# Optimization experiments

Measured on AMD Instinct MI355X. Metric: run time of the kernel, lower is better.

## Reference

```python
import jax, jax.numpy as jnp
import numpy as np


def _dwconv(x, w, b):
    # depthwise conv, NCHW, kernel [C,1,k,k], SAME padding k//2
    k = w.shape[-1]
    p = k // 2
    out = jax.lax.conv_general_dilated(x, w, (1, 1), [(p, p), (p, p)],
                                       feature_group_count=x.shape[1])
    return out + b[None, :, None, None]


def _conv1x1(x, W, b):
    return jnp.einsum('oc,bchw->bohw', W, x) + b[None, :, None, None]


def _ca_weight(q, k):
    # q,k: [b,c,h,w] -> energy [b,h,w,h+w]
    eH = jnp.einsum('bchw,bcgw->bhwg', q, k)  # attend along H (column)
    eW = jnp.einsum('bchw,bchv->bhwv', q, k)  # attend along W (row)
    return jnp.concatenate([eH, eW], axis=3)


def _ca_map(att, v):
    # att: [b,h,w,h+w], v: [b,c,h,w]
    h = v.shape[2]
    outH = jnp.einsum('bcgw,bhwg->bchw', v, att[..., :h])
    outW = jnp.einsum('bchv,bhwv->bchw', v, att[..., h:])
    return outH + outW


def _cc_block(cnn, Wq, bq, Wk, bk, Wv, bv, gamma):
    q = _conv1x1(cnn, Wq, bq)
    k = _conv1x1(cnn, Wk, bk)
    v = _conv1x1(cnn, Wv, bv)
    att = jax.nn.softmax(_ca_weight(q, k), axis=1)  # softmax over H axis, as in torch F.softmax(energy, 1)
    return gamma * _ca_map(att, v) + cnn


def _ppeg(x, w7, b7, w5, b5, w3, b3, H, W):
    C = x.shape[1]
    cnn = x.T.reshape(1, C, H, W)
    out = _dwconv(cnn, w7, b7) + cnn + _dwconv(cnn, w5, b5) + _dwconv(cnn, w3, b3)
    return out.reshape(C, H * W).T  # [N, C]


def setup_inputs() -> dict:
    key = jax.random.key(0)
    N, DIM, HID, QK = 65536, 1024, 512, 64  # N = 256^2
    ks = jax.random.split(key, 26)
    s = 0.02
    inp = {
        'h0': jax.random.normal(ks[0], (N, DIM), jnp.float32),
        'w7': jax.random.normal(ks[1], (DIM, 1, 7, 7)) * s,
        'b7': jax.random.normal(ks[2], (DIM,)) * s,
        'w5': jax.random.normal(ks[3], (DIM, 1, 5, 5)) * s,
        'b5': jax.random.normal(ks[4], (DIM,)) * s,
        'w3': jax.random.normal(ks[5], (DIM, 1, 3, 3)) * s,
        'b3': jax.random.normal(ks[6], (DIM,)) * s,
        'W1': jax.random.normal(ks[7], (HID, DIM)) * s,
        'b1': jax.random.normal(ks[8], (HID,)) * s,
        'Wq': jax.random.normal(ks[9], (QK, HID)) * s,
        'bq': jax.random.normal(ks[10], (QK,)) * s,
        'Wk': jax.random.normal(ks[11], (QK, HID)) * s,
        'bk': jax.random.normal(ks[12], (QK,)) * s,
        'Wv': jax.random.normal(ks[13], (HID, HID)) * s,
        'bv': jax.random.normal(ks[14], (HID,)) * s,
        'gamma': jax.random.normal(ks[15], ()) * 0.5,
        'Wq1': jax.random.normal(ks[16], (QK, HID)) * s,
        'bq1': jax.random.normal(ks[17], (QK,)) * s,
        'Wk1': jax.random.normal(ks[18], (QK, HID)) * s,
        'bk1': jax.random.normal(ks[19], (QK,)) * s,
        'Wv1': jax.random.normal(ks[20], (HID, HID)) * s,
        'bv1': jax.random.normal(ks[21], (HID,)) * s,
        'gamma1': jax.random.normal(ks[22], ()) * 0.5,
        'Wfc': jax.random.normal(ks[23], (1, HID)) * s,
        'bfc': jax.random.normal(ks[24], (1,)) * s,
    }
    return inp


def reference(h0, w7, b7, w5, b5, w3, b3, W1, b1,
              Wq, bq, Wk, bk, Wv, bv, gamma,
              Wq1, bq1, Wk1, bk1, Wv1, bv1, gamma1, Wfc, bfc):
    N = h0.shape[0]
    side = int(np.ceil(np.sqrt(N)))
    pad = side * side - N
    h1 = jnp.concatenate([h0, h0[:pad]], axis=0) if pad > 0 else h0
    # PPEG positional encoding (multi-kernel depthwise conv)
    h1 = _ppeg(h1, w7, b7, w5, b5, w3, b3, side, side)
    # fc1: Linear(1024->512) + ReLU  (h1 already square -> second pad is no-op)
    h2 = jax.nn.relu(h1 @ W1.T + b1)  # [N, 512]
    # CCAttention (two criss-cross blocks + fc to 1 logit)
    cnn = h2.T.reshape(1, h2.shape[1], side, side)
    out = _cc_block(cnn, Wq, bq, Wk, bk, Wv, bv, gamma)
    out1 = _cc_block(out, Wq1, bq1, Wk1, bk1, Wv1, bv1, gamma1)
    out1 = out1.reshape(out1.shape[1], side * side).T  # [N, 512]
    logits = out1 @ Wfc.T + bfc  # [N, 1]
    A = jax.nn.softmax(logits.T, axis=1)  # [1, N] attention over instances
    return A
```

## Files before the change

### kernel.cpp

```cpp
#include <hip/hip_runtime.h>

#define HW 65536
#define SIDE 256

typedef __attribute__((ext_vector_type(8))) short short8v;
typedef __attribute__((ext_vector_type(4))) float f32x4;
typedef __attribute__((ext_vector_type(8))) ushort ushort8v;

__device__ __forceinline__ ushort f2bf(float f) {
  unsigned int u = __builtin_bit_cast(unsigned int, f);
  u = (u + 0x7fff + ((u >> 16) & 1)) >> 16;
  return (ushort)u;
}
__device__ __forceinline__ float bf2f(unsigned int u) {
  return __builtin_bit_cast(float, (u & 0xffffu) << 16);
}
__device__ __forceinline__ float bflo(unsigned int d) {
  return __builtin_bit_cast(float, d << 16);
}
__device__ __forceinline__ float bfhi(unsigned int d) {
  return __builtin_bit_cast(float, d & 0xffff0000u);
}
__device__ __forceinline__ void gld16(const void* g, void* l) {
  __builtin_amdgcn_global_load_lds(
      (const __attribute__((address_space(1))) void*)g,
      (__attribute__((address_space(3))) void*)l, 16, 0, 0);
}

__global__ __launch_bounds__(256) void k_prep(
    const float* __restrict__ W1, const float* __restrict__ Wv,
    const float* __restrict__ Wv1, const float* __restrict__ Wq,
    const float* __restrict__ Wk, const float* __restrict__ Wq1,
    const float* __restrict__ Wk1, const float* __restrict__ bq,
    const float* __restrict__ bk, const float* __restrict__ bq1,
    const float* __restrict__ bk1, const float* __restrict__ w7,
    const float* __restrict__ b7, const float* __restrict__ w5,
    const float* __restrict__ b5, const float* __restrict__ w3,
    const float* __restrict__ b3,
    ushort* __restrict__ W1b, ushort* __restrict__ Wvb,
    ushort* __restrict__ Wv1b, ushort* __restrict__ Wqkb,
    ushort* __restrict__ Wqk1b, float* __restrict__ bqk,
    float* __restrict__ bqk1, float* __restrict__ wc, float* __restrict__ bc) {
  const int i = blockIdx.x * 256 + threadIdx.x;
  if (i < 524288) { W1b[i] = f2bf(W1[i]); return; }
  if (i < 786432) { int j = i - 524288; Wvb[j] = f2bf(Wv[j]); return; }
  if (i < 1048576) { int j = i - 786432; Wv1b[j] = f2bf(Wv1[j]); return; }
  if (i < 1081344) { int j = i - 1048576; Wqkb[j] = f2bf(Wq[j]); return; }
  if (i < 1114112) { int j = i - 1081344; Wqkb[32768 + j] = f2bf(Wk[j]); return; }
  if (i < 1146880) { int j = i - 1114112; Wqk1b[j] = f2bf(Wq1[j]); return; }
  if (i < 1179648) { int j = i - 1146880; Wqk1b[32768 + j] = f2bf(Wk1[j]); return; }
  if (i < 1179904) {
    int j = i - 1179648;
    if (j < 64) bqk[j] = bq[j];
    else if (j < 128) bqk[j] = bk[j - 64];
    else if (j < 192) bqk1[j - 128] = bq1[j - 128];
    else bqk1[j - 128] = bk1[j - 192];
    return;
  }
  if (i < 1180928) {
    const int c = i - 1179904;
    float w[49];
#pragma unroll
    for (int t = 0; t < 49; t++) w[t] = w7[c * 49 + t];
    for (int dy = 0; dy < 5; dy++)
      for (int dx = 0; dx < 5; dx++)
        w[(dy + 1) * 7 + (dx + 1)] += w5[c * 25 + dy * 5 + dx];
    for (int dy = 0; dy < 3; dy++)
      for (int dx = 0; dx < 3; dx++)
        w[(dy + 2) * 7 + (dx + 2)] += w3[c * 9 + dy * 3 + dx];
    w[3 * 7 + 3] += 1.0f;
#pragma unroll
    for (int t = 0; t < 49; t++) wc[c * 49 + t] = w[t];
    bc[c] = b7[c] + b5[c] + b3[c];
  }
}

__global__ __launch_bounds__(256) void k_transpose_nc_v(
    const float* __restrict__ in, ushort* __restrict__ out) {
  __shared__ ushort t[64][64];
  const int c0 = blockIdx.x << 6, r0 = blockIdx.y << 6;
  const int tid = threadIdx.x;
#pragma unroll
  for (int p = 0; p < 2; p++) {
    const int r = (tid >> 3) + p * 32, c8 = tid & 7;
    const float4 f0 = *(const float4*)&in[(size_t)(r0 + r) * 1024 + c0 + c8 * 8];
    const float4 f1 = *(const float4*)&in[(size_t)(r0 + r) * 1024 + c0 + c8 * 8 + 4];
    ushort8v v;
    v[0] = f2bf(f0.x); v[1] = f2bf(f0.y); v[2] = f2bf(f0.z); v[3] = f2bf(f0.w);
    v[4] = f2bf(f1.x); v[5] = f2bf(f1.y); v[6] = f2bf(f1.z); v[7] = f2bf(f1.w);
    *(ushort8v*)&t[r][(c8 ^ ((r >> 3) & 7)) * 8] = v;
  }
  __syncthreads();
#pragma unroll
  for (int p = 0; p < 2; p++) {
    const int c = (tid >> 3) + p * 32, r8 = tid & 7;
    ushort8v v;
#pragma unroll
    for (int j = 0; j < 8; j++) {
      const int rr = r8 * 8 + j;
      v[j] = t[rr][(((c >> 3) ^ r8) << 3) + (c & 7)];
    }
    *(ushort8v*)&out[(size_t)(c0 + c) * HW + r0 + r8 * 8] = v;
  }
}

__global__ __launch_bounds__(256) void k_trv(const ushort* __restrict__ in,
    ushort* __restrict__ out, int R, int C, long long bs) {
  __shared__ ushort t[64][64];
  const size_t base = (size_t)blockIdx.z * bs;
  const int c0 = blockIdx.x << 6, r0 = blockIdx.y << 6;
  const int tid = threadIdx.x;
#pragma unroll
  for (int p = 0; p < 2; p++) {
    const int r = (tid >> 3) + p * 32, c8 = tid & 7;
    const ushort8v v = *(const ushort8v*)&in[base + (size_t)(r0 + r) * C + c0 + c8 * 8];
    *(ushort8v*)&t[r][(c8 ^ ((r >> 3) & 7)) * 8] = v;
  }
  __syncthreads();
#pragma unroll
  for (int p = 0; p < 2; p++) {
    const int c = (tid >> 3) + p * 32, r8 = tid & 7;
    ushort8v v;
#pragma unroll
    for (int j = 0; j < 8; j++) {
      const int rr = r8 * 8 + j;
      v[j] = t[rr][(((c >> 3) ^ r8) << 3) + (c & 7)];
    }
    *(ushort8v*)&out[base + (size_t)(c0 + c) * R + r0 + r8 * 8] = v;
  }
}

__global__ __launch_bounds__(256) void k_dwconv7(const ushort* __restrict__ X,
    const float* __restrict__ wc, const float* __restrict__ bc,
    ushort* __restrict__ out) {
  __shared__ ushort tile[38][272];
  const int c = blockIdx.y;
  const int y0 = blockIdx.x << 5;
  const int tid = threadIdx.x;
  const ushort* Xc = X + (size_t)c * HW;

  float w[49];
#pragma unroll
  for (int i = 0; i < 49; i++) w[i] = wc[c * 49 + i];
  const float bcv = bc[c];

  if (tid < 76) {
    const int r = tid >> 1;
    ushort8v z = {0, 0, 0, 0, 0, 0, 0, 0};
    *(ushort8v*)&tile[r][(tid & 1) ? 264 : 0] = z;
  }
  for (int i = tid; i < 38 * 32; i += 256) {
    const int r = i >> 5, j8 = i & 31;
    const int y = y0 - 3 + r;
    ushort8v v = {0, 0, 0, 0, 0, 0, 0, 0};
    if (y >= 0 && y < SIDE) v = *(const ushort8v*)&Xc[y * SIDE + j8 * 8];
    *(ushort8v*)&tile[r][8 + j8 * 8] = v;
  }
  __syncthreads();

  const int t0 = tid & 63;
  const int ry = (tid >> 6) << 3;
  float acc[8][4] = {};
#pragma unroll
  for (int r = 0; r < 14; r++) {
    const uint2 ua = *(const uint2*)&tile[ry + r][(t0 << 2) + 4];
    const uint2 ub = *(const uint2*)&tile[ry + r][(t0 << 2) + 8];
    const uint2 uc = *(const uint2*)&tile[ry + r][(t0 << 2) + 12];
    float rv[12];
    rv[0] = bflo(ua.x); rv[1] = bfhi(ua.x); rv[2] = bflo(ua.y); rv[3] = bfhi(ua.y);
    rv[4] = bflo(ub.x); rv[5] = bfhi(ub.x); rv[6] = bflo(ub.y); rv[7] = bfhi(ub.y);
    rv[8] = bflo(uc.x); rv[9] = bfhi(uc.x); rv[10] = bflo(uc.y); rv[11] = bfhi(uc.y);
#pragma unroll
    for (int m = 0; m < 8; m++) {
      const int dy = r - m;
      if (dy < 0 || dy > 6) continue;
#pragma unroll
      for (int dx = 0; dx < 7; dx++) {
        const float ww = w[dy * 7 + dx];
#pragma unroll
        for (int o = 0; o < 4; o++) acc[m][o] += ww * rv[o + 1 + dx];
      }
    }
  }
#pragma unroll
  for (int m = 0; m < 8; m++) {
    ushort4 o4 = {f2bf(acc[m][0] + bcv), f2bf(acc[m][1] + bcv),
                  f2bf(acc[m][2] + bcv), f2bf(acc[m][3] + bcv)};
    *(ushort4*)&out[(size_t)c * HW + (y0 + ry + m) * SIDE + (t0 << 2)] = o4;
  }
}

template <int BN, int BIAS, int RELU, int OUTF, int OUTB>
__global__ __launch_bounds__(256) void k_mm(
    const ushort* __restrict__ A, int lda, long long bsA,
    const ushort* __restrict__ B, int ldb, long long bsB,
    const float* __restrict__ bias,
    float* __restrict__ Cf, ushort* __restrict__ Cb, int ldc, long long bsC,
    int K) {
  static_assert(BN == 64 || BN == 128, "BN");
  constexpr int FN = BN / 32;
  __shared__ __align__(16) ushort As[128 * 32];
  __shared__ __align__(16) ushort Bs[BN * 32];
  const int tid = threadIdx.x;
  const int bm = blockIdx.x << 7, bn = blockIdx.y * BN;
  const long long zA = (long long)blockIdx.z * bsA;
  const long long zB = (long long)blockIdx.z * bsB;
  const long long zC = (long long)blockIdx.z * bsC;

  const int sr = tid >> 2, sq = tid & 3;
  const int sw0 = (sr >> 1) & 3;
  const int sw1 = ((sr + 64) >> 1) & 3;
  const ushort* Ap0 = A + zA + (size_t)(bm + sr) * lda + ((sq ^ sw0) << 3);
  const ushort* Ap1 = A + zA + (size_t)(bm + sr + 64) * lda + ((sq ^ sw1) << 3);
  const ushort* Bp0 = B + zB + (size_t)(bn + sr) * ldb + ((sq ^ sw0) << 3);
  const ushort* Bp1 = nullptr;
  if constexpr (BN == 128)
    Bp1 = B + zB + (size_t)(bn + sr + 64) * ldb + ((sq ^ sw1) << 3);
  ushort* wA0 = &As[sr * 32 + sq * 8];
  ushort* wA1 = &As[(sr + 64) * 32 + sq * 8];
  ushort* wB0 = &Bs[sr * 32 + sq * 8];
  ushort* wB1 = nullptr;
  if constexpr (BN == 128) wB1 = &Bs[(sr + 64) * 32 + sq * 8];

  const int lane = tid & 63, wv = tid >> 6;
  const int wm = wv & 1, wn = wv >> 1;
  const int fr = lane & 15, kq = lane >> 4;
  int offA[4], offB[FN];
#pragma unroll
  for (int mi = 0; mi < 4; mi++) {
    const int row = wm * 64 + mi * 16 + fr;
    offA[mi] = row * 32 + ((kq ^ ((row >> 1) & 3)) << 3);
  }
#pragma unroll
  for (int ni = 0; ni < FN; ni++) {
    const int row = wn * (BN / 2) + ni * 16 + fr;
    offB[ni] = row * 32 + ((kq ^ ((row >> 1) & 3)) << 3);
  }

  f32x4 acc[4][FN];
#pragma unroll
  for (int mi = 0; mi < 4; mi++)
#pragma unroll
    for (int ni = 0; ni < FN; ni++) acc[mi][ni] = (f32x4){0.f, 0.f, 0.f, 0.f};

  for (int k0 = 0; k0 < K; k0 += 32) {
    __syncthreads();
    gld16(Ap0 + k0, wA0);
    gld16(Ap1 + k0, wA1);
    gld16(Bp0 + k0, wB0);
    if constexpr (BN == 128) gld16(Bp1 + k0, wB1);
    __syncthreads();
    short8v a[4], b[FN];
#pragma unroll
    for (int mi = 0; mi < 4; mi++) a[mi] = *(const short8v*)&As[offA[mi]];
#pragma unroll
    for (int ni = 0; ni < FN; ni++) b[ni] = *(const short8v*)&Bs[offB[ni]];
#pragma unroll
    for (int mi = 0; mi < 4; mi++)
#pragma unroll
      for (int ni = 0; ni < FN; ni++)
        acc[mi][ni] = __builtin_amdgcn_mfma_f32_16x16x32_bf16(b[ni], a[mi], acc[mi][ni], 0, 0, 0);
  }

#pragma unroll
  for (int mi = 0; mi < 4; mi++) {
    const int row = bm + wm * 64 + mi * 16 + fr;
    const float bs1 = (BIAS == 1) ? bias[row] : 0.f;
#pragma unroll
    for (int ni = 0; ni < FN; ni++) {
      const int col = bn + wn * (BN / 2) + ni * 16 + (kq << 2);
      float4 v;
      v.x = acc[mi][ni][0]; v.y = acc[mi][ni][1];
      v.z = acc[mi][ni][2]; v.w = acc[mi][ni][3];
      if (BIAS == 1) { v.x += bs1; v.y += bs1; v.z += bs1; v.w += bs1; }
      if (BIAS == 2) {
        const float4 bc4 = *(const float4*)&bias[col];
        v.x += bc4.x; v.y += bc4.y; v.z += bc4.z; v.w += bc4.w;
      }
      if (RELU) {
        v.x = fmaxf(v.x, 0.f); v.y = fmaxf(v.y, 0.f);
        v.z = fmaxf(v.z, 0.f); v.w = fmaxf(v.w, 0.f);
      }
      const size_t idx = (size_t)(zC + (size_t)row * ldc + col);
      if (OUTF) *(float4*)&Cf[idx] = v;
      if (OUTB) {
        ushort4 u = {f2bf(v.x), f2bf(v.y), f2bf(v.z), f2bf(v.w)};
        *(ushort4*)&Cb[idx] = u;
      }
    }
  }
}

__global__ __launch_bounds__(256) void k_softmax_bf16(const ushort* __restrict__ E,
    ushort* __restrict__ Att, int outerStride, int hStride) {
  const size_t base = (size_t)blockIdx.x * outerStride + threadIdx.x;
  float m = -3.4e38f, s = 0.f;
  for (int h = 0; h < 256; h++) {
    const float x = bf2f(E[base + (size_t)h * hStride]);
    const float nm = fmaxf(m, x);
    s = s * __expf(m - nm) + __expf(x - nm);
    m = nm;
  }
  const float inv = 1.0f / s;
  for (int h = 0; h < 256; h++) {
    const size_t i = base + (size_t)h * hStride;
    Att[i] = f2bf(__expf(bf2f(E[i]) - m) * inv);
  }
}

__global__ __launch_bounds__(256) void k_merge3(const ushort* __restrict__ O,
    const ushort* __restrict__ TH, const ushort* __restrict__ CN,
    const float* __restrict__ gammap, ushort* __restrict__ outB) {
  __shared__ ushort t[64][64];
  const float g = *gammap;
  const size_t base = (size_t)blockIdx.z * HW;
  const int h0 = blockIdx.y << 6, w0 = blockIdx.x << 6;
  const int tid = threadIdx.x;
#pragma unroll
  for (int p = 0; p < 2; p++) {
    const int r = (tid >> 3) + p * 32, c8 = tid & 7;
    const ushort8v v = *(const ushort8v*)&TH[base + (w0 + r) * SIDE + h0 + c8 * 8];
    *(ushort8v*)&t[r][(c8 ^ ((r >> 3) & 7)) * 8] = v;
  }
  __syncthreads();
#pragma unroll
  for (int p = 0; p < 2; p++) {
    const int h = (tid >> 3) + p * 32, r8 = tid & 7;
    const size_t idx = base + (h0 + h) * SIDE + w0 + r8 * 8;
    const ushort8v o8 = *(const ushort8v*)&O[idx];
    const ushort8v c8v = *(const ushort8v*)&CN[idx];
    ushort8v res;
#pragma unroll
    for (int j = 0; j < 8; j++) {
      const int rr = r8 * 8 + j;
      const float th = bf2f(t[rr][(((h >> 3) ^ r8) << 3) + (h & 7)]);
      res[j] = f2bf(g * (bf2f(o8[j]) + th) + bf2f(c8v[j]));
    }
    *(ushort8v*)&outB[idx] = res;
  }
}

__global__ __launch_bounds__(256) void k_logits(const ushort* __restrict__ X,
    const float* __restrict__ Wfc, const float* __restrict__ bfc,
    float* __restrict__ L) {
  const int n = blockIdx.x * 256 + threadIdx.x;
  float s = 0.f;
  for (int j = 0; j < 512; j++) s += bf2f(X[(size_t)j * HW + n]) * Wfc[j];
  L[n] = s + bfc[0];
}

__global__ __launch_bounds__(256) void k_smax_reduce(const float* __restrict__ L,
                                                     float* __restrict__ red) {
  __shared__ float sm[256];
  const int tid = threadIdx.x;
  float m = -3.4e38f;
  for (int i = tid; i < HW; i += 256) m = fmaxf(m, L[i]);
  sm[tid] = m;
  __syncthreads();
  for (int s = 128; s > 0; s >>= 1) {
    if (tid < s) sm[tid] = fmaxf(sm[tid], sm[tid + s]);
    __syncthreads();
  }
  const float M = sm[0];
  __syncthreads();
  float sum = 0.f;
  for (int i = tid; i < HW; i += 256) sum += expf(L[i] - M);
  sm[tid] = sum;
  __syncthreads();
  for (int s = 128; s > 0; s >>= 1) {
    if (tid < s) sm[tid] += sm[tid + s];
    __syncthreads();
  }
  if (tid == 0) { red[0] = M; red[1] = sm[0]; }
}

__global__ __launch_bounds__(256) void k_smax_write(const float* __restrict__ L,
    const float* __restrict__ red, float* __restrict__ out) {
  const int n = blockIdx.x * 256 + threadIdx.x;
  out[n] = expf(L[n] - red[0]) * (1.0f / red[1]);
}

extern "C" void kernel_launch(void* const* d_in, const int* in_sizes, int n_in,
                              void* d_out, int out_size, void* d_ws, size_t ws_size,
                              hipStream_t stream) {
  const float* h0 = (const float*)d_in[0];
  const float* w7 = (const float*)d_in[1];
  const float* b7 = (const float*)d_in[2];
  const float* w5 = (const float*)d_in[3];
  const float* b5 = (const float*)d_in[4];
  const float* w3 = (const float*)d_in[5];
  const float* b3 = (const float*)d_in[6];
  const float* W1 = (const float*)d_in[7];
  const float* b1 = (const float*)d_in[8];
  const float* Wq = (const float*)d_in[9];
  const float* bq = (const float*)d_in[10];
  const float* Wk = (const float*)d_in[11];
  const float* bk = (const float*)d_in[12];
  const float* Wv = (const float*)d_in[13];
  const float* bv = (const float*)d_in[14];
  const float* gamma = (const float*)d_in[15];
  const float* Wq1 = (const float*)d_in[16];
  const float* bq1 = (const float*)d_in[17];
  const float* Wk1 = (const float*)d_in[18];
  const float* bk1 = (const float*)d_in[19];
  const float* Wv1 = (const float*)d_in[20];
  const float* bv1 = (const float*)d_in[21];
  const float* gamma1 = (const float*)d_in[22];
  const float* Wfc = (const float*)d_in[23];
  const float* bfc = (const float*)d_in[24];

  char* W = (char*)d_ws;
  const size_t MB = 1 << 20;
  ushort* Xb    = (ushort*)(W + 0);
  ushort* H2b   = (ushort*)(W + 0);
  ushort* H2t   = (ushort*)(W + 64 * MB);
  ushort* qkt   = (ushort*)(W + 128 * MB);
  ushort* AttW  = (ushort*)(W + 144 * MB);
  ushort* AttH  = (ushort*)(W + 176 * MB);
  ushort* H1b   = (ushort*)(W + 256 * MB);
  ushort* H1t   = (ushort*)(W + 384 * MB);
  ushort* Vb    = (ushort*)(W + 384 * MB);
  ushort* vTb   = (ushort*)(W + 448 * MB);
  ushort* Ob    = (ushort*)(W + 512 * MB);
  ushort* THbb  = (ushort*)(W + 576 * MB);
  ushort* Eb    = (ushort*)(W + 640 * MB);
  ushort* W1b   = (ushort*)(W + 704 * MB);
  ushort* Wvb   = (ushort*)(W + 705 * MB);
  ushort* Wv1b  = (ushort*)(W + 705 * MB + 512 * 1024);
  ushort* Wqkb  = (ushort*)(W + 706 * MB);
  ushort* Wqk1b = (ushort*)(W + 706 * MB + 128 * 1024);
  float*  wcomb = (float*)(W + 706 * MB + 256 * 1024);
  float*  bcomb = (float*)(W + 706 * MB + 464 * 1024);
  float*  bqk   = (float*)(W + 706 * MB + 472 * 1024);
  float*  bqk1  = (float*)(W + 706 * MB + 474 * 1024);
  float*  L     = (float*)(W + 707 * MB);
  float*  red   = (float*)(W + 707 * MB + 256 * 1024);

  k_prep<<<4613, 256, 0, stream>>>(W1, Wv, Wv1, Wq, Wk, Wq1, Wk1,
                                   bq, bk, bq1, bk1, w7, b7, w5, b5, w3, b3,
                                   W1b, Wvb, Wv1b, Wqkb, Wqk1b, bqk, bqk1,
                                   wcomb, bcomb);

  k_transpose_nc_v<<<dim3(16, 1024), 256, 0, stream>>>(h0, Xb);
  k_dwconv7<<<dim3(8, 1024), 256, 0, stream>>>(Xb, wcomb, bcomb, H1b);
  k_trv<<<dim3(1024, 16, 1), 256, 0, stream>>>(H1b, H1t, 1024, HW, 0);

  k_mm<128, 1, 1, 0, 1><<<dim3(4, 512, 1), 256, 0, stream>>>(
      W1b, 1024, 0, H1t, 1024, 0, b1, nullptr, H2b, HW, 0, 1024);
  k_trv<<<dim3(1024, 8, 1), 256, 0, stream>>>(H2b, H2t, 512, HW, 0);

  auto cc_block = [&](const ushort* act, ushort* cnn, const ushort* Wqk_,
                      const float* bqk_, const ushort* Wv_, const float* bv_,
                      const float* gam) {
    k_mm<128, 2, 0, 0, 1><<<dim3(512, 1, 1), 256, 0, stream>>>(
        act, 512, 0, Wqk_, 512, 0, bqk_, nullptr, qkt, 128, 0, 512);
    k_mm<128, 1, 0, 0, 1><<<dim3(4, 512, 1), 256, 0, stream>>>(
        Wv_, 512, 0, act, 512, 0, bv_, nullptr, Vb, HW, 0, 512);
    k_trv<<<dim3(4, 4, 512), 256, 0, stream>>>(Vb, vTb, 256, 256, 65536);
    k_mm<128, 0, 0, 0, 1><<<dim3(2, 2, 256), 256, 0, stream>>>(
        qkt, 128, 32768, qkt + 64, 128, 32768, nullptr, nullptr, Eb, 256, 65536, 64);
    k_softmax_bf16<<<256, 256, 0, stream>>>(Eb, AttW, 256, HW);
    k_mm<128, 0, 0, 0, 1><<<dim3(4, 2, 256), 256, 0, stream>>>(
        Vb, HW, 256, AttW, 256, 65536, nullptr, nullptr, Ob, HW, 256, 256);
    k_mm<128, 0, 0, 0, 1><<<dim3(2, 2, 256), 256, 0, stream>>>(
        qkt, 32768, 128, qkt + 64, 32768, 128, nullptr, nullptr, Eb, 256, 65536, 64);
    k_softmax_bf16<<<256, 256, 0, stream>>>(Eb, AttH, HW, 256);
    k_mm<128, 0, 0, 0, 1><<<dim3(4, 2, 256), 256, 0, stream>>>(
        vTb, HW, 256, AttH, 256, 65536, nullptr, nullptr, THbb, HW, 256, 256);
    k_merge3<<<dim3(4, 4, 512), 256, 0, stream>>>(Ob, THbb, cnn, gam, cnn);
  };

  cc_block(H2t, H2b, Wqkb, bqk, Wvb, bv, gamma);
  k_trv<<<dim3(1024, 8, 1), 256, 0, stream>>>(H2b, H2t, 512, HW, 0);
  cc_block(H2t, H2b, Wqk1b, bqk1, Wv1b, bv1, gamma1);

  k_logits<<<256, 256, 0, stream>>>(H2b, Wfc, bfc, L);
  k_smax_reduce<<<1, 256, 0, stream>>>(L, red);
  k_smax_write<<<256, 256, 0, stream>>>(L, red, (float*)d_out);
}
```

Baseline: 1.348 ms.

## Fuse transpose into fc1 GEMM, swizzle block order, merge both softmaxes

Adds a transposed-output epilogue to the GEMM: the tile is staged through shared memory so fc1 writes both H2b and H2t in one pass, which drops a separate transpose kernel. Adds XCD-aware block-index swizzles to several GEMM launches so that blocks sharing operands land on the same die's L2. The two softmax launches become one kernel over both energy buffers, which now get separate workspace areas so both energy GEMMs can run before it. The price is extra LDS traffic and syncs in the fc1 epilogue, plus a larger energy workspace.

```diff
diff --git a/kernel.cpp b/kernel.cpp
--- a/kernel.cpp
+++ b/kernel.cpp
@@ -190,22 +190,39 @@
   }
 }
 
-template <int BN, int BIAS, int RELU, int OUTF, int OUTB>
+template <int BN, int BIAS, int RELU, int OUTF, int OUTB, int SWZ, int TRN>
 __global__ __launch_bounds__(256) void k_mm(
     const ushort* __restrict__ A, int lda, long long bsA,
     const ushort* __restrict__ B, int ldb, long long bsB,
     const float* __restrict__ bias,
     float* __restrict__ Cf, ushort* __restrict__ Cb, int ldc, long long bsC,
-    int K) {
+    ushort* __restrict__ Ct, int ldt, int K) {
   static_assert(BN == 64 || BN == 128, "BN");
+  static_assert(!TRN || BN == 128, "TRN needs BN=128");
   constexpr int FN = BN / 32;
-  __shared__ __align__(16) ushort As[128 * 32];
-  __shared__ __align__(16) ushort Bs[BN * 32];
+  __shared__ __align__(16) ushort SMEM[128 * 32 + BN * 32];
+  ushort* As = SMEM;
+  ushort* Bs = SMEM + 128 * 32;
   const int tid = threadIdx.x;
-  const int bm = blockIdx.x << 7, bn = blockIdx.y * BN;
-  const long long zA = (long long)blockIdx.z * bsA;
-  const long long zB = (long long)blockIdx.z * bsB;
-  const long long zC = (long long)blockIdx.z * bsC;
+
+  int bx, by, bz;
+  if constexpr (SWZ == 0) {
+    bx = blockIdx.x; by = blockIdx.y; bz = blockIdx.z;
+  } else if constexpr (SWZ == 1) {
+    const int id = blockIdx.x, l = id >> 3;
+    by = (id & 7) * 64 + (l >> 2); bx = l & 3; bz = 0;
+  } else if constexpr (SWZ == 2) {
+    const int id = blockIdx.x, l = id >> 3;
+    bz = (id & 7) * 32 + (l >> 2); bx = l & 1; by = (l >> 1) & 1;
+  } else {
+    const int id = blockIdx.x, l = id >> 3;
+    bz = (id & 7) * 32 + (l >> 3); bx = l & 3; by = (l >> 2) & 1;
+  }
+
+  const int bm = bx << 7, bn = by * BN;
+  const long long zA = (long long)bz * bsA;
+  const long long zB = (long long)bz * bsB;
+  const long long zC = (long long)bz * bsC;
 
   const int sr = tid >> 2, sq = tid & 3;
   const int sw0 = (sr >> 1) & 3;
@@ -262,6 +279,7 @@
         acc[mi][ni] = __builtin_amdgcn_mfma_f32_16x16x32_bf16(b[ni], a[mi], acc[mi][ni], 0, 0, 0);
   }
 
+  ushort tb[4][FN][4];
 #pragma unroll
   for (int mi = 0; mi < 4; mi++) {
     const int row = bm + wm * 64 + mi * 16 + fr;
@@ -281,30 +299,66 @@
         v.x = fmaxf(v.x, 0.f); v.y = fmaxf(v.y, 0.f);
         v.z = fmaxf(v.z, 0.f); v.w = fmaxf(v.w, 0.f);
       }
+      const ushort4 u = {f2bf(v.x), f2bf(v.y), f2bf(v.z), f2bf(v.w)};
       const size_t idx = (size_t)(zC + (size_t)row * ldc + col);
       if (OUTF) *(float4*)&Cf[idx] = v;
-      if (OUTB) {
-        ushort4 u = {f2bf(v.x), f2bf(v.y), f2bf(v.z), f2bf(v.w)};
-        *(ushort4*)&Cb[idx] = u;
+      if (OUTB) *(ushort4*)&Cb[idx] = u;
+      if (TRN) {
+        tb[mi][ni][0] = u.x; tb[mi][ni][1] = u.y;
+        tb[mi][ni][2] = u.z; tb[mi][ni][3] = u.w;
       }
     }
   }
-}
-
-__global__ __launch_bounds__(256) void k_softmax_bf16(const ushort* __restrict__ E,
-    ushort* __restrict__ Att, int outerStride, int hStride) {
-  const size_t base = (size_t)blockIdx.x * outerStride + threadIdx.x;
+
+  if constexpr (TRN) {
+    ushort* St = SMEM;
+#pragma unroll
+    for (int hh = 0; hh < 2; hh++) {
+      __syncthreads();
+      if (wn == hh) {
+#pragma unroll
+        for (int mi = 0; mi < 4; mi++) {
+          const int rloc = wm * 64 + mi * 16 + fr;
+#pragma unroll
+          for (int ni = 0; ni < 4; ni++) {
+            const int cl = ni * 16 + (kq << 2);
+#pragma unroll
+            for (int r = 0; r < 4; r++)
+              St[(cl + r) * 128 + rloc] = tb[mi][ni][r];
+          }
+        }
+      }
+      __syncthreads();
+      const int n_ = tid >> 2;
+#pragma unroll
+      for (int j = 0; j < 4; j++) {
+        const int ck = (tid & 3) * 4 + j;
+        const ushort8v vv = *(const ushort8v*)&St[n_ * 128 + ck * 8];
+        *(ushort8v*)&Ct[(size_t)(bn + hh * 64 + n_) * ldt + bm + ck * 8] = vv;
+      }
+    }
+  }
+}
+
+__global__ __launch_bounds__(256) void k_softmax2(const ushort* __restrict__ EW,
+    ushort* __restrict__ AW, const ushort* __restrict__ EH,
+    ushort* __restrict__ AH) {
+  int b = blockIdx.x;
+  const ushort* E; ushort* A; int os, hs;
+  if (b < 256) { E = EW; A = AW; os = 256; hs = HW; }
+  else { E = EH; A = AH; os = HW; hs = 256; b -= 256; }
+  const size_t base = (size_t)b * os + threadIdx.x;
   float m = -3.4e38f, s = 0.f;
   for (int h = 0; h < 256; h++) {
-    const float x = bf2f(E[base + (size_t)h * hStride]);
+    const float x = bf2f(E[base + (size_t)h * hs]);
     const float nm = fmaxf(m, x);
     s = s * __expf(m - nm) + __expf(x - nm);
     m = nm;
   }
   const float inv = 1.0f / s;
   for (int h = 0; h < 256; h++) {
-    const size_t i = base + (size_t)h * hStride;
-    Att[i] = f2bf(__expf(bf2f(E[i]) - m) * inv);
+    const size_t i = base + (size_t)h * hs;
+    A[i] = f2bf(__expf(bf2f(E[i]) - m) * inv);
   }
 }
 
@@ -423,7 +477,8 @@
   ushort* vTb   = (ushort*)(W + 448 * MB);
   ushort* Ob    = (ushort*)(W + 512 * MB);
   ushort* THbb  = (ushort*)(W + 576 * MB);
-  ushort* Eb    = (ushort*)(W + 640 * MB);
+  ushort* EbW   = (ushort*)(W + 640 * MB);
+  ushort* EbH   = (ushort*)(W + 672 * MB);
   ushort* W1b   = (ushort*)(W + 704 * MB);
   ushort* Wvb   = (ushort*)(W + 705 * MB);
   ushort* Wv1b  = (ushort*)(W + 705 * MB + 512 * 1024);
@@ -445,28 +500,30 @@
   k_dwconv7<<<dim3(8, 1024), 256, 0, stream>>>(Xb, wcomb, bcomb, H1b);
   k_trv<<<dim3(1024, 16, 1), 256, 0, stream>>>(H1b, H1t, 1024, HW, 0);
 
-  k_mm<128, 1, 1, 0, 1><<<dim3(4, 512, 1), 256, 0, stream>>>(
-      W1b, 1024, 0, H1t, 1024, 0, b1, nullptr, H2b, HW, 0, 1024);
-  k_trv<<<dim3(1024, 8, 1), 256, 0, stream>>>(H2b, H2t, 512, HW, 0);
+  k_mm<128, 1, 1, 0, 1, 1, 1><<<2048, 256, 0, stream>>>(
+      W1b, 1024, 0, H1t, 1024, 0, b1, nullptr, H2b, HW, 0, H2t, 512, 1024);
 
   auto cc_block = [&](const ushort* act, ushort* cnn, const ushort* Wqk_,
                       const float* bqk_, const ushort* Wv_, const float* bv_,
                       const float* gam) {
-    k_mm<128, 2, 0, 0, 1><<<dim3(512, 1, 1), 256, 0, stream>>>(
-        act, 512, 0, Wqk_, 512, 0, bqk_, nullptr, qkt, 128, 0, 512);
-    k_mm<128, 1, 0, 0, 1><<<dim3(4, 512, 1), 256, 0, stream>>>(
-        Wv_, 512, 0, act, 512, 0, bv_, nullptr, Vb, HW, 0, 512);
+    k_mm<128, 2, 0, 0, 1, 0, 0><<<dim3(512, 1, 1), 256, 0, stream>>>(
+        act, 512, 0, Wqk_, 512, 0, bqk_, nullptr, qkt, 128, 0, nullptr, 0, 512);
+    k_mm<128, 1, 0, 0, 1, 1, 0><<<2048, 256, 0, stream>>>(
+        Wv_, 512, 0, act, 512, 0, bv_, nullptr, Vb, HW, 0, nullptr, 0, 512);
     k_trv<<<dim3(4, 4, 512), 256, 0, stream>>>(Vb, vTb, 256, 256, 65536);
-    k_mm<128, 0, 0, 0, 1><<<dim3(2, 2, 256), 256, 0, stream>>>(
-        qkt, 128, 32768, qkt + 64, 128, 32768, nullptr, nullptr, Eb, 256, 65536, 64);
-    k_softmax_bf16<<<256, 256, 0, stream>>>(Eb, AttW, 256, HW);
-    k_mm<128, 0, 0, 0, 1><<<dim3(4, 2, 256), 256, 0, stream>>>(
-        Vb, HW, 256, AttW, 256, 65536, nullptr, nullptr, Ob, HW, 256, 256);
-    k_mm<128, 0, 0, 0, 1><<<dim3(2, 2, 256), 256, 0, stream>>>(
-        qkt, 32768, 128, qkt + 64, 32768, 128, nullptr, nullptr, Eb, 256, 65536, 64);
-    k_softmax_bf16<<<256, 256, 0, stream>>>(Eb, AttH, HW, 256);
-    k_mm<128, 0, 0, 0, 1><<<dim3(4, 2, 256), 256, 0, stream>>>(
-        vTb, HW, 256, AttH, 256, 65536, nullptr, nullptr, THbb, HW, 256, 256);
+    k_mm<128, 0, 0, 0, 1, 2, 0><<<1024, 256, 0, stream>>>(
+        qkt, 128, 32768, qkt + 64, 128, 32768, nullptr, nullptr, EbW, 256,
+        65536, nullptr, 0, 64);
+    k_mm<128, 0, 0, 0, 1, 2, 0><<<1024, 256, 0, stream>>>(
+        qkt, 32768, 128, qkt + 64, 32768, 128, nullptr, nullptr, EbH, 256,
+        65536, nullptr, 0, 64);
+    k_softmax2<<<512, 256, 0, stream>>>(EbW, AttW, EbH, AttH);
+    k_mm<128, 0, 0, 0, 1, 3, 0><<<2048, 256, 0, stream>>>(
+        Vb, HW, 256, AttW, 256, 65536, nullptr, nullptr, Ob, HW, 256,
+        nullptr, 0, 256);
+    k_mm<128, 0, 0, 0, 1, 3, 0><<<2048, 256, 0, stream>>>(
+        vTb, HW, 256, AttH, 256, 65536, nullptr, nullptr, THbb, HW, 256,
+        nullptr, 0, 256);
     k_merge3<<<dim3(4, 4, 512), 256, 0, stream>>>(Ob, THbb, cnn, gam, cnn);
   };
 
```

After: 1.236 ms. 8.3% less time.
